# Optimization experiments

Measured on AMD Instinct MI355X. Metric: run time of the kernel, lower is better.

Reference implementation:

```python
import jax, jax.numpy as jnp
import numpy as np
import math

B, T, D = 4, 2048, 1024
N, D_OUT = 1024, 1024
EPS_A = 1e-4
PROJ_BOUND = 1.0


def setup_inputs() -> dict:
    key = jax.random.key(0)
    ks = jax.random.split(key, 4)
    # reset_parameters: rho=0.99, delta0=1.0
    rho, delta0 = 0.99, 1.0
    alpha0 = -math.log(rho) / delta0
    alpha_log_val = math.log(math.expm1(alpha0))
    delta_bias_val = math.log(math.expm1(delta0))
    return {
        "u": jax.random.normal(ks[0], (B, T, D), dtype=jnp.float32),
        "z0": jnp.zeros((B, N), dtype=jnp.float32),
        "W_in_raw": 0.02 * jax.random.normal(ks[1], (N, D), dtype=jnp.float32),
        "W_out_raw": 0.02 * jax.random.normal(ks[2], (D_OUT, N), dtype=jnp.float32),
        "pn_w": 0.02 * jax.random.normal(ks[3], (3 * N, D), dtype=jnp.float32),
        "pn_b": jnp.zeros((3 * N,), dtype=jnp.float32),
        "alpha_log": jnp.full((N,), alpha_log_val, dtype=jnp.float32),
        "delta_bias": jnp.full((N,), delta_bias_val, dtype=jnp.float32),
        "log_gamma": jnp.float32(0.0),
    }


def _bounded_linear(x, W, bound):
    # y = x @ (W/scale)^T with ||W/scale||_2 <= bound (exact spectral norm)
    sigma = jnp.maximum(jnp.linalg.norm(W, ord=2), 1e-5)
    scale = jnp.maximum(sigma / bound, 1.0)
    return x @ (W / scale).T


def reference(u, z0, W_in_raw, W_out_raw, pn_w, pn_b, alpha_log, delta_bias, log_gamma):
    g = jnp.exp(log_gamma)
    u_scaled = g * _bounded_linear(u, W_in_raw, PROJ_BOUND)        # (B,T,N)
    raw = u @ pn_w.T + pn_b                                        # (B,T,3N)
    delta_raw, b_raw, c_raw = jnp.split(raw, 3, axis=-1)
    delta = jax.nn.softplus(delta_raw + delta_bias)
    alpha = jax.nn.softplus(alpha_log)                             # (N,)
    a = jnp.minimum(jnp.exp(-delta * alpha), 1.0 - EPS_A)          # (B,T,N)
    b = jnp.tanh(b_raw)
    c = jnp.tanh(c_raw)
    # exact spectral norm of [[a,b],[c,0]] per coordinate
    p = a * a + c * c
    r = b * b
    q = a * b
    disc = (p - r) * (p - r) + 4.0 * q * q
    lam_max = 0.5 * (p + r + jnp.sqrt(disc + 1e-12))
    sigma = jnp.sqrt(lam_max + 1e-12)
    scale = jnp.maximum(sigma, 1.0)
    a, b, c = a / scale, b / scale, c / scale
    # diagonal recurrence z_{t+1} = a_t * z_t + b_t * u_scaled_t via associative scan
    bu = b * u_scaled
    bu = bu.at[:, 0].add(a[:, 0] * z0)
    def combine(x, y):
        a1, b1 = x
        a2, b2 = y
        return (a2 * a1, a2 * b1 + b2)
    _, z_next = jax.lax.associative_scan(combine, (a, bu), axis=1)  # z_1..z_T (B,T,N)
    # y_t = W_out (c_t * z_t) with z_t = state BEFORE update (one-step delay)
    states = jnp.concatenate([z0[:, None, :], z_next[:, :-1, :]], axis=1)  # z_0..z_{T-1}
    y_hat = c * states
    y = _bounded_linear(y_hat, W_out_raw, PROJ_BOUND)              # (B,T,D_out)
    return y
```

## Files before the change

### kernel.cpp

```cpp
#include <hip/hip_runtime.h>
#include <stdint.h>

#define B_ 4
#define T_ 2048
#define D_ 1024
#define N_ 1024
#define TC 32
#define NCH (T_/TC)
#define SQN 8

typedef __attribute__((ext_vector_type(4))) float f32x4;
typedef __attribute__((ext_vector_type(8))) short bf16x8;
typedef __attribute__((ext_vector_type(4))) unsigned short us4;

__device__ __forceinline__ unsigned short f2bf(float f){
  unsigned int u = __float_as_uint(f);
  return (unsigned short)((u + 0x7fffu + ((u >> 16) & 1u)) >> 16);
}
__device__ __forceinline__ float bf2f(unsigned short h){
  return __uint_as_float(((unsigned int)h) << 16);
}

#define U4    2097152
#define WIN4   262144
#define PNW4   786432
#define WOUT4  262144
#define CONV_BLOCKS ((U4 + WIN4 + PNW4 + WOUT4 + 255)/256)

__global__ void k_convert_all(const float* __restrict__ u, const float* __restrict__ Win,
                              const float* __restrict__ pnw, const float* __restrict__ Wout,
                              unsigned short* __restrict__ u16, unsigned short* __restrict__ Wcat16,
                              unsigned short* __restrict__ Wout16, float* __restrict__ sc){
  if (blockIdx.x == 0 && threadIdx.x < 64) sc[threadIdx.x] = 0.f;
  long i = (long)blockIdx.x * 256 + threadIdx.x;
  const float* src; unsigned short* dst; long o;
  if (i < U4)                      { src = u;    dst = u16;               o = i; }
  else if (i < U4+WIN4)            { src = Win;  dst = Wcat16;            o = i - U4; }
  else if (i < U4+WIN4+PNW4)       { src = pnw;  dst = Wcat16 + 1048576;  o = i - (U4+WIN4); }
  else if (i < U4+WIN4+PNW4+WOUT4) { src = Wout; dst = Wout16;            o = i - (U4+WIN4+PNW4); }
  else return;
  float4 v = ((const float4*)src)[o];
  us4 w;
  w.x = f2bf(v.x); w.y = f2bf(v.y); w.z = f2bf(v.z); w.w = f2bf(v.w);
  ((us4*)dst)[o] = w;
}

__device__ __forceinline__ void load_lds16(const unsigned short* g, unsigned short* l){
  __builtin_amdgcn_global_load_lds((const __attribute__((address_space(1))) void*)g,
                                   (__attribute__((address_space(3))) void*)l, 16, 0, 0);
}

template<int OUTBF16>
__global__ __launch_bounds__(256) void k_gemm(
    const unsigned short* __restrict__ A,
    const unsigned short* __restrict__ Bmat,
    void* __restrict__ C0,
    int M, int N, int K,
    const float* __restrict__ sc, int step)
{
  __shared__ alignas(16) unsigned short As[128*64];
  __shared__ alignas(16) unsigned short Bs[128*64];
  const int tid = threadIdx.x;
  const int wid = tid >> 6;
  const int lane = tid & 63;
  const int bn = blockIdx.x, bm = blockIdx.y;

  char* C = (char*)C0;
  float outscale = (step >= 0) ? sc[step] : 1.f;

  const int wr = wid >> 1, wc = wid & 1;
  const int rg = lane >> 3;
  const int cby = (lane & 7) << 4;
  const int srow0 = wid * 32;
  const int frow = lane & 15;
  const int kgrp = lane >> 4;

  const size_t Abase = (size_t)bm * 128 * K;
  const size_t Bbase = (size_t)bn * 128 * K;

  f32x4 acc[4][4] = {};

  for (int kt = 0; kt < K; kt += 64){
    #pragma unroll
    for (int i = 0; i < 4; i++){
      int r = srow0 + i*8 + rg;
      int cb = cby ^ ((r & 7) << 4);
      load_lds16(A    + Abase + (size_t)r*K + kt + (cb >> 1), As + (srow0 + i*8)*64);
      load_lds16(Bmat + Bbase + (size_t)r*K + kt + (cb >> 1), Bs + (srow0 + i*8)*64);
    }
    __syncthreads();
    #pragma unroll
    for (int kk = 0; kk < 2; kk++){
      const int kbyte = kk*64 + kgrp*16;
      bf16x8 af[4], bfv[4];
      #pragma unroll
      for (int m = 0; m < 4; m++){
        int r = wr*64 + m*16 + frow;
        af[m] = *(const bf16x8*)((const char*)As + r*128 + (kbyte ^ ((r & 7) << 4)));
      }
      #pragma unroll
      for (int n2 = 0; n2 < 4; n2++){
        int r = wc*64 + n2*16 + frow;
        bfv[n2] = *(const bf16x8*)((const char*)Bs + r*128 + (kbyte ^ ((r & 7) << 4)));
      }
      #pragma unroll
      for (int m = 0; m < 4; m++)
        #pragma unroll
        for (int n2 = 0; n2 < 4; n2++)
          acc[m][n2] = __builtin_amdgcn_mfma_f32_16x16x32_bf16(af[m], bfv[n2], acc[m][n2], 0, 0, 0);
    }
    __syncthreads();
  }

  const int row0 = bm*128 + wr*64;
  const int col0 = bn*128 + wc*64 + frow;
  #pragma unroll
  for (int m = 0; m < 4; m++){
    #pragma unroll
    for (int n2 = 0; n2 < 4; n2++){
      const int col = col0 + n2*16;
      const int rb = row0 + m*16 + kgrp*4;
      #pragma unroll
      for (int j = 0; j < 4; j++){
        float v = acc[m][n2][j] * outscale;
        if (OUTBF16) ((unsigned short*)C)[(size_t)(rb + j)*N + col] = f2bf(v);
        else         ((float*)C)[(size_t)(rb + j)*N + col] = v;
      }
    }
  }
}

__global__ __launch_bounds__(256) void k_sq(
    const unsigned short* __restrict__ A0, unsigned short* __restrict__ C0,
    const unsigned short* __restrict__ A1, unsigned short* __restrict__ C1,
    float* __restrict__ sc, int step)
{
  __shared__ alignas(16) unsigned short As0[64*128], Bs0[64*128];
  __shared__ alignas(16) unsigned short As1[64*128], Bs1[64*128];
  const int tid = threadIdx.x;
  const int wid = tid >> 6;
  const int lane = tid & 63;
  const int bn = blockIdx.x, bm = blockIdx.y, z = blockIdx.z;

  const unsigned short* A = z ? A1 : A0;
  unsigned short* C = z ? C1 : C0;
  float outscale = 1.f;
  if (step > 0){ float t = sc[8 + (step-1)*2 + z]; outscale = 1.f/(t*t); }

  const int wr = wid >> 1, wc = wid & 1;
  const int frow = lane & 15;
  const int kgrp = lane >> 4;

  const int srl = lane >> 4;
  const int sgr = lane & 15;
  const int swzr = wid*4 + srl;
  const int scol_e = ((sgr ^ swzr) << 3);

  const size_t Arow = (size_t)bm * 64;
  const size_t Brow = (size_t)bn * 64;

  f32x4 acc[2][2] = {};

  auto stage = [&](unsigned short* as, unsigned short* bs, int t){
    const int kt = t * 128;
    #pragma unroll
    for (int i = 0; i < 4; i++){
      int r = i*16 + wid*4 + srl;
      load_lds16(A + (Arow + r)*1024 + kt + scol_e, as + (i*16 + wid*4)*128);
      load_lds16(A + (Brow + r)*1024 + kt + scol_e, bs + (i*16 + wid*4)*128);
    }
  };

  auto compute = [&](const unsigned short* as, const unsigned short* bs){
    #pragma unroll
    for (int ks = 0; ks < 4; ks++){
      const int kb = ks*64 + kgrp*16;
      bf16x8 af[2], bfv[2];
      #pragma unroll
      for (int m = 0; m < 2; m++){
        int r = wr*32 + m*16 + frow;
        af[m] = *(const bf16x8*)((const char*)as + r*256 + (kb ^ (frow << 4)));
      }
      #pragma unroll
      for (int n2 = 0; n2 < 2; n2++){
        int r = wc*32 + n2*16 + frow;
        bfv[n2] = *(const bf16x8*)((const char*)bs + r*256 + (kb ^ (frow << 4)));
      }
      #pragma unroll
      for (int m = 0; m < 2; m++)
        #pragma unroll
        for (int n2 = 0; n2 < 2; n2++)
          acc[m][n2] = __builtin_amdgcn_mfma_f32_16x16x32_bf16(af[m], bfv[n2], acc[m][n2], 0, 0, 0);
    }
  };

  stage(As0, Bs0, 0);
  __syncthreads();
  for (int t2 = 0; t2 < 8; t2 += 2){
    if (t2 + 1 < 8) stage(As1, Bs1, t2 + 1);
    compute(As0, Bs0);
    __syncthreads();
    if (t2 + 2 < 8) stage(As0, Bs0, t2 + 2);
    compute(As1, Bs1);
    __syncthreads();
  }

  const int row0 = bm*64 + wr*32;
  const int col0 = bn*64 + wc*32 + frow;
  float fr = 0.f;
  #pragma unroll
  for (int m = 0; m < 2; m++){
    #pragma unroll
    for (int n2 = 0; n2 < 2; n2++){
      const int col = col0 + n2*16;
      const int rb = row0 + m*16 + kgrp*4;
      #pragma unroll
      for (int j = 0; j < 4; j++){
        float v = acc[m][n2][j] * outscale;
        C[(size_t)(rb + j)*1024 + col] = f2bf(v);
        fr += v*v;
      }
    }
  }
  if (bm == bn && wr == wc){
    int j = frow - kgrp*4;
    if (j >= 0 && j < 4){
      float d = (acc[0][0][j] + acc[1][1][j]) * outscale;
      atomicAdd(&sc[8 + step*2 + z], d);
    }
  }
  if (step == SQN){
    #pragma unroll
    for (int off = 32; off; off >>= 1) fr += __shfl_down(fr, off, 64);
    if (lane == 0) atomicAdd(&sc[8 + 2*(SQN+1) + z], fr);
  }
}

__global__ void k_final(float* sc){
  int z = threadIdx.x;
  if (z < 2){
    float ll = 0.f, w = 1.f, t = 1.f;
    for (int i = 0; i <= SQN; i++){
      t = sc[8 + 2*i + z];
      ll += w * __logf(t);
      w *= 0.5f;
    }
    float tlast = sc[8 + 2*(SQN+1) + z] / (t*t);
    ll += w * __logf(tlast);
    float sig = __expf(0.5f * ll);
    sig = fmaxf(sig, 1e-5f);
    sc[z] = 1.f / fmaxf(sig, 1.f);
  }
}

__device__ __forceinline__ float softplusf(float x){
  return (x > 0.f) ? (x + __logf(1.f + __expf(-x))) : __logf(1.f + __expf(x));
}
__device__ __forceinline__ float tanhfastf(float x){
  float e = __expf(2.f * x);
  return 1.f - 2.f/(e + 1.f);
}
__device__ __forceinline__ void abc_from(float pin, float draw, float braw, float craw,
    float alpha, float ginv, float& a_o, float& bu_o, float& c_o){
  float sp = softplusf(draw);
  float av = __expf(-sp * alpha);
  av = fminf(av, 1.f - 1e-4f);
  float bv = tanhfastf(braw);
  float cv = tanhfastf(craw);
  float p = av*av + cv*cv;
  float r = bv*bv;
  float q = av*bv;
  float pr = p - r;
  float disc = pr*pr + 4.f*q*q;
  float lam = 0.5f*(p + r + sqrtf(disc + 1e-12f));
  float sig = sqrtf(lam + 1e-12f);
  float inv = 1.f / fmaxf(sig, 1.f);
  a_o = av * inv;
  c_o = cv * inv;
  bu_o = (bv * inv) * (pin * ginv);
}

__global__ __launch_bounds__(256) void k_pass1(
    const unsigned short* __restrict__ P,
    const float* __restrict__ alog, const float* __restrict__ dbias,
    const float* __restrict__ pnb, const float* __restrict__ lgam,
    const float* __restrict__ sc,
    float* __restrict__ Asum, float* __restrict__ Ssum)
{
  const int tid = threadIdx.x;
  const int n0 = blockIdx.y*512 + tid*2;
  const int ch = blockIdx.x, b = blockIdx.z;
  const float ginv = __expf(lgam[0]) * sc[0];
  float alpha[2], bd[2], bb[2], bc[2], A[2], S[2];
  #pragma unroll
  for (int j = 0; j < 2; j++){
    alpha[j] = softplusf(alog[n0+j]);
    bd[j] = dbias[n0+j] + pnb[n0+j];
    bb[j] = pnb[N_ + n0+j];
    bc[j] = pnb[2*N_ + n0+j];
    A[j] = 1.f; S[j] = 0.f;
  }
  const unsigned short* Pr = P + (size_t)(b*T_ + ch*TC) * (4*N_);
  #pragma unroll 4
  for (int i = 0; i < TC; i++){
    unsigned int vp = *(const unsigned int*)(Pr + n0);
    unsigned int vd = *(const unsigned int*)(Pr + N_ + n0);
    unsigned int vb = *(const unsigned int*)(Pr + 2*N_ + n0);
    unsigned int vc = *(const unsigned int*)(Pr + 3*N_ + n0);
    #pragma unroll
    for (int j = 0; j < 2; j++){
      float pin  = bf2f((unsigned short)(j ? (vp>>16) : (vp & 0xffffu)));
      float draw = bf2f((unsigned short)(j ? (vd>>16) : (vd & 0xffffu))) + bd[j];
      float braw = bf2f((unsigned short)(j ? (vb>>16) : (vb & 0xffffu))) + bb[j];
      float craw = bf2f((unsigned short)(j ? (vc>>16) : (vc & 0xffffu))) + bc[j];
      float a, bu, c;
      abc_from(pin, draw, braw, craw, alpha[j], ginv, a, bu, c);
      S[j] = fmaf(a, S[j], bu);
      A[j] *= a;
    }
    Pr += 4*N_;
  }
  const size_t idx = (size_t)(b*NCH + ch)*N_ + n0;
  Asum[idx] = A[0]; Asum[idx+1] = A[1];
  Ssum[idx] = S[0]; Ssum[idx+1] = S[1];
}

__global__ void k_pass2(const float* __restrict__ Asum, const float* __restrict__ Ssum,
                        const float* __restrict__ z0, float* __restrict__ Zent)
{
  const int n = blockIdx.x*256 + threadIdx.x;
  const int b = blockIdx.y;
  float z = z0[b*N_ + n];
  for (int ch = 0; ch < NCH; ch++){
    const size_t idx = (size_t)(b*NCH + ch)*N_ + n;
    Zent[idx] = z;
    z = fmaf(Asum[idx], z, Ssum[idx]);
  }
}

__global__ __launch_bounds__(256) void k_pass3(
    const unsigned short* __restrict__ P,
    const float* __restrict__ alog, const float* __restrict__ dbias,
    const float* __restrict__ pnb, const float* __restrict__ lgam,
    const float* __restrict__ sc, const float* __restrict__ Zent,
    unsigned short* __restrict__ yh)
{
  const int tid = threadIdx.x;
  const int n0 = blockIdx.y*512 + tid*2;
  const int ch = blockIdx.x, b = blockIdx.z;
  const float ginv = __expf(lgam[0]) * sc[0];
  float alpha[2], bd[2], bb[2], bc[2], z[2];
  #pragma unroll
  for (int j = 0; j < 2; j++){
    alpha[j] = softplusf(alog[n0+j]);
    bd[j] = dbias[n0+j] + pnb[n0+j];
    bb[j] = pnb[N_ + n0+j];
    bc[j] = pnb[2*N_ + n0+j];
  }
  const size_t zidx = (size_t)(b*NCH + ch)*N_ + n0;
  z[0] = Zent[zidx]; z[1] = Zent[zidx+1];
  const unsigned short* Pr = P + (size_t)(b*T_ + ch*TC) * (4*N_);
  unsigned short* Y = yh + (size_t)(b*T_ + ch*TC)*N_ + n0;
  #pragma unroll 4
  for (int i = 0; i < TC; i++){
    unsigned int vp = *(const unsigned int*)(Pr + n0);
    unsigned int vd = *(const unsigned int*)(Pr + N_ + n0);
    unsigned int vb = *(const unsigned int*)(Pr + 2*N_ + n0);
    unsigned int vc = *(const unsigned int*)(Pr + 3*N_ + n0);
    unsigned int ow = 0;
    #pragma unroll
    for (int j = 0; j < 2; j++){
      float pin  = bf2f((unsigned short)(j ? (vp>>16) : (vp & 0xffffu)));
      float draw = bf2f((unsigned short)(j ? (vd>>16) : (vd & 0xffffu))) + bd[j];
      float braw = bf2f((unsigned short)(j ? (vb>>16) : (vb & 0xffffu))) + bb[j];
      float craw = bf2f((unsigned short)(j ? (vc>>16) : (vc & 0xffffu))) + bc[j];
      float a, bu, c;
      abc_from(pin, draw, braw, craw, alpha[j], ginv, a, bu, c);
      float yv = c * z[j];
      z[j] = fmaf(a, z[j], bu);
      ow |= ((unsigned int)f2bf(yv)) << (16*j);
    }
    *(unsigned int*)Y = ow;
    Y += N_;
    Pr += 4*N_;
  }
}

extern "C" void kernel_launch(void* const* d_in, const int* in_sizes, int n_in,
                              void* d_out, int out_size, void* d_ws, size_t ws_size,
                              hipStream_t stream)
{
  const float* u    = (const float*)d_in[0];
  const float* z0   = (const float*)d_in[1];
  const float* Win  = (const float*)d_in[2];
  const float* Wout = (const float*)d_in[3];
  const float* pnw  = (const float*)d_in[4];
  const float* pnb  = (const float*)d_in[5];
  const float* alog = (const float*)d_in[6];
  const float* dbias= (const float*)d_in[7];
  const float* lgam = (const float*)d_in[8];

  char* ws = (char*)d_ws;
  size_t off = 0;
  auto alloc = [&](size_t bytes) -> void* {
    void* p = ws + off;
    off += (bytes + 255) & ~(size_t)255;
    return p;
  };
  float*          sc     = (float*)         alloc(1024);
  unsigned short* u16    = (unsigned short*)alloc((size_t)8192*1024*2);
  unsigned short* Wcat16 = (unsigned short*)alloc((size_t)4096*1024*2);
  unsigned short* Wout16 = (unsigned short*)alloc((size_t)1024*1024*2);
  unsigned short* P16    = (unsigned short*)alloc((size_t)8192*4096*2);
  unsigned short* yh16   = (unsigned short*)alloc((size_t)8192*1024*2);
  unsigned short* Hping  = (unsigned short*)alloc((size_t)2*1024*1024*2);
  unsigned short* Hpong  = (unsigned short*)alloc((size_t)2*1024*1024*2);
  float*          Asum   = (float*)alloc((size_t)B_*NCH*N_*4);
  float*          Ssum   = (float*)alloc((size_t)B_*NCH*N_*4);
  float*          Zent   = (float*)alloc((size_t)B_*NCH*N_*4);

  k_convert_all<<<CONV_BLOCKS, 256, 0, stream>>>(u, Win, pnw, Wout, u16, Wcat16, Wout16, sc);

  dim3 gsq(16, 16, 2);
  k_sq<<<gsq, 256, 0, stream>>>(Wcat16, Hping, Wout16, Hping + (size_t)1024*1024, sc, 0);
  unsigned short* hin = Hping;
  unsigned short* hout = Hpong;
  for (int s = 1; s <= SQN; s++){
    k_sq<<<gsq, 256, 0, stream>>>(hin, hout, hin + (size_t)1024*1024, hout + (size_t)1024*1024, sc, s);
    unsigned short* t = hin; hin = hout; hout = t;
  }
  k_final<<<1, 64, 0, stream>>>(sc);

  dim3 g1(4096/128, 8192/128, 1);
  k_gemm<1><<<g1, 256, 0, stream>>>(u16, Wcat16, P16, 8192, 4096, 1024, sc, -1);

  dim3 gp1(NCH, N_/512, B_);
  k_pass1<<<gp1, 256, 0, stream>>>(P16, alog, dbias, pnb, lgam, sc, Asum, Ssum);
  dim3 gp2(N_/256, B_);
  k_pass2<<<gp2, 256, 0, stream>>>(Asum, Ssum, z0, Zent);
  k_pass3<<<gp1, 256, 0, stream>>>(P16, alog, dbias, pnb, lgam, sc, Zent, yh16);

  dim3 g2(1024/128, 8192/128, 1);
  k_gemm<0><<<g2, 256, 0, stream>>>(yh16, Wout16, d_out, 8192, 1024, 1024, sc, 1);
}
```

Baseline: 320.9 us.

## Add 256x256-tile pipelined bf16 GEMM for the input projection

Replaces the generic 128x128 GEMM for the large u @ [W_in; pn_w]^T projection with a dedicated kernel using 256x256 tiles, 512 threads, and a 4-stage LDS ring fed by direct global-to-LDS loads with XOR swizzling. Loads for future k-tiles are interleaved between split MFMA phases, with priority raised around MFMA bursts. The aim is more data reuse per tile and better overlap of memory with compute. It hardcodes K=1024 and an output stride of 4096, no longer applies the scale argument (the old call passed step -1), and uses heavy register and LDS budgets.

After: 332.5 us. 3.6% more time.

```diff
diff --git a/kernel.cpp b/kernel.cpp
--- a/kernel.cpp
+++ b/kernel.cpp
@@ -48,6 +48,132 @@
 __device__ __forceinline__ void load_lds16(const unsigned short* g, unsigned short* l){
   __builtin_amdgcn_global_load_lds((const __attribute__((address_space(1))) void*)g,
                                    (__attribute__((address_space(3))) void*)l, 16, 0, 0);
+}
+
+__global__ __launch_bounds__(512, 2) void k_pgemm(
+    const unsigned short* __restrict__ A,
+    const unsigned short* __restrict__ Bmat,
+    unsigned short* __restrict__ C)
+{
+  __shared__ alignas(16) unsigned short As[4][256*32];
+  __shared__ alignas(16) unsigned short Bs[4][256*32];
+  const int tid = threadIdx.x;
+  const int wid = tid >> 6;
+  const int lane = tid & 63;
+  const int bn = blockIdx.x, bm = blockIdx.y;
+
+  const int wr = wid >> 2;
+  const int wc = wid & 3;
+  const int frow = lane & 15;
+  const int kgrp = lane >> 4;
+
+  const int srow = lane >> 2;
+  const int sgr  = lane & 3;
+
+  f32x4 acc[8][4] = {};
+
+  const unsigned short* Ab = A + (size_t)bm * 256 * 1024;
+  const unsigned short* Bb = Bmat + (size_t)bn * 256 * 1024;
+
+  auto stageA = [&](int t){
+    const int p = t & 3;
+    #pragma unroll
+    for (int l = 0; l < 2; l++){
+      int r = (wid*2 + l)*16 + srow;
+      int g = sgr ^ ((r >> 1) & 3);
+      load_lds16(Ab + (size_t)r*1024 + t*32 + g*8, &As[p][(wid*2 + l)*512]);
+    }
+  };
+  auto stageB = [&](int t){
+    const int p = t & 3;
+    #pragma unroll
+    for (int l = 0; l < 2; l++){
+      int r = (wid*2 + l)*16 + srow;
+      int g = sgr ^ ((r >> 1) & 3);
+      load_lds16(Bb + (size_t)r*1024 + t*32 + g*8, &Bs[p][(wid*2 + l)*512]);
+    }
+  };
+
+  stageA(0); stageB(0);
+  stageA(1); stageB(1);
+  stageA(2); stageB(2);
+  asm volatile("s_waitcnt vmcnt(8)" ::: "memory");
+  __builtin_amdgcn_s_barrier();
+
+  bf16x8 bfv[4];
+
+  auto tile_body = [&](int t, bool doStage){
+    const int p = t & 3;
+    bf16x8 afv[4];
+    #pragma unroll
+    for (int m = 0; m < 4; m++){
+      int r = wr*128 + m*16 + frow;
+      int g = kgrp ^ ((r >> 1) & 3);
+      afv[m] = *(const bf16x8*)&As[p][r*32 + g*8];
+    }
+    #pragma unroll
+    for (int n = 0; n < 4; n++){
+      int r = wc*64 + n*16 + frow;
+      int g = kgrp ^ ((r >> 1) & 3);
+      bfv[n] = *(const bf16x8*)&Bs[p][r*32 + g*8];
+    }
+    if (doStage) stageA(t + 3);
+    __builtin_amdgcn_s_barrier();
+    asm volatile("s_waitcnt lgkmcnt(0)" ::: "memory");
+    __builtin_amdgcn_sched_barrier(0);
+    __builtin_amdgcn_s_setprio(1);
+    #pragma unroll
+    for (int m = 0; m < 4; m++)
+      #pragma unroll
+      for (int n = 0; n < 4; n++)
+        acc[m][n] = __builtin_amdgcn_mfma_f32_16x16x32_bf16(afv[m], bfv[n], acc[m][n], 0, 0, 0);
+    __builtin_amdgcn_s_setprio(0);
+    __builtin_amdgcn_s_barrier();
+    #pragma unroll
+    for (int m = 0; m < 4; m++){
+      int r = wr*128 + (m+4)*16 + frow;
+      int g = kgrp ^ ((r >> 1) & 3);
+      afv[m] = *(const bf16x8*)&As[p][r*32 + g*8];
+    }
+    if (doStage) stageB(t + 3);
+    __builtin_amdgcn_s_barrier();
+    asm volatile("s_waitcnt lgkmcnt(0)" ::: "memory");
+    __builtin_amdgcn_sched_barrier(0);
+    __builtin_amdgcn_s_setprio(1);
+    #pragma unroll
+    for (int m = 0; m < 4; m++)
+      #pragma unroll
+      for (int n = 0; n < 4; n++)
+        acc[m+4][n] = __builtin_amdgcn_mfma_f32_16x16x32_bf16(afv[m], bfv[n], acc[m+4][n], 0, 0, 0);
+    __builtin_amdgcn_s_setprio(0);
+  };
+
+  for (int t = 0; t < 29; t++){
+    tile_body(t, true);
+    asm volatile("s_waitcnt vmcnt(8)" ::: "memory");
+    __builtin_amdgcn_s_barrier();
+  }
+  tile_body(29, false);
+  asm volatile("s_waitcnt vmcnt(4)" ::: "memory");
+  __builtin_amdgcn_s_barrier();
+  tile_body(30, false);
+  asm volatile("s_waitcnt vmcnt(0)" ::: "memory");
+  __builtin_amdgcn_s_barrier();
+  tile_body(31, false);
+
+  const int row0 = bm*256 + wr*128;
+  const int col0 = bn*256 + wc*64 + frow;
+  #pragma unroll
+  for (int m = 0; m < 8; m++){
+    #pragma unroll
+    for (int n = 0; n < 4; n++){
+      const int col = col0 + n*16;
+      const int rb = row0 + m*16 + kgrp*4;
+      #pragma unroll
+      for (int j = 0; j < 4; j++)
+        C[(size_t)(rb + j)*4096 + col] = f2bf(acc[m][n][j]);
+    }
+  }
 }
 
 template<int OUTBF16>
@@ -431,8 +557,8 @@
   }
   k_final<<<1, 64, 0, stream>>>(sc);
 
-  dim3 g1(4096/128, 8192/128, 1);
-  k_gemm<1><<<g1, 256, 0, stream>>>(u16, Wcat16, P16, 8192, 4096, 1024, sc, -1);
+  dim3 gP(4096/256, 8192/256);
+  k_pgemm<<<gP, 512, 0, stream>>>(u16, Wcat16, P16);
 
   dim3 gp1(NCH, N_/512, B_);
   k_pass1<<<gp1, 256, 0, stream>>>(P16, alog, dbias, pnb, lgam, sc, Asum, Ssum);
@@ -440,6 +566,6 @@
   k_pass2<<<gp2, 256, 0, stream>>>(Asum, Ssum, z0, Zent);
   k_pass3<<<gp1, 256, 0, stream>>>(P16, alog, dbias, pnb, lgam, sc, Zent, yh16);
 
-  dim3 g2(1024/128, 8192/128, 1);
+  dim3 g2(1024/128, 8192/128);
   k_gemm<0><<<g2, 256, 0, stream>>>(yh16, Wout16, d_out, 8192, 1024, 1024, sc, 1);
 }
```

## Fuse squaring chain and scan tail into persistent kernels with grid barriers

Applied to the files above, without the earlier changes.

Replaces the nine per-step squaring launches and the k_final launch with one persistent 512-block kernel. The steps inside it are separated by a software grid barrier built on an atomic counter. The three scan passes and the output GEMM are likewise merged into one 512-block kernel with grid barriers between phases. The goal is to remove kernel launch gaps and tail effects. In exchange it relies on all 512 blocks being co-resident, spin-waits on atomics, and runs the output GEMM inside the tail kernel rather than as a separate tuned launch.

Result: slower. 1.216 ms (+278.8%).

```diff
diff --git a/kernel.cpp b/kernel.cpp
--- a/kernel.cpp
+++ b/kernel.cpp
@@ -21,6 +21,18 @@
   return __uint_as_float(((unsigned int)h) << 16);
 }
 
+__device__ __forceinline__ void gsync(unsigned* bar, unsigned target){
+  __syncthreads();
+  if (threadIdx.x == 0){
+    __threadfence();
+    atomicAdd(bar, 1u);
+    while (__hip_atomic_load(bar, __ATOMIC_ACQUIRE, __HIP_MEMORY_SCOPE_AGENT) < target)
+      __builtin_amdgcn_s_sleep(2);
+    __threadfence();
+  }
+  __syncthreads();
+}
+
 #define U4    2097152
 #define WIN4   262144
 #define PNW4   786432
@@ -31,7 +43,7 @@
                               const float* __restrict__ pnw, const float* __restrict__ Wout,
                               unsigned short* __restrict__ u16, unsigned short* __restrict__ Wcat16,
                               unsigned short* __restrict__ Wout16, float* __restrict__ sc){
-  if (blockIdx.x == 0 && threadIdx.x < 64) sc[threadIdx.x] = 0.f;
+  if (blockIdx.x == 0 && threadIdx.x < 128) sc[threadIdx.x] = 0.f;
   long i = (long)blockIdx.x * 256 + threadIdx.x;
   const float* src; unsigned short* dst; long o;
   if (i < U4)                      { src = u;    dst = u16;               o = i; }
@@ -130,126 +142,133 @@
   }
 }
 
-__global__ __launch_bounds__(256) void k_sq(
-    const unsigned short* __restrict__ A0, unsigned short* __restrict__ C0,
-    const unsigned short* __restrict__ A1, unsigned short* __restrict__ C1,
-    float* __restrict__ sc, int step)
+__global__ __launch_bounds__(256) void k_chain(
+    const unsigned short* __restrict__ W0,
+    const unsigned short* __restrict__ W1,
+    unsigned short* __restrict__ Hp,
+    unsigned short* __restrict__ Hq,
+    float* sc, unsigned* bar)
 {
   __shared__ alignas(16) unsigned short As0[64*128], Bs0[64*128];
   __shared__ alignas(16) unsigned short As1[64*128], Bs1[64*128];
   const int tid = threadIdx.x;
   const int wid = tid >> 6;
   const int lane = tid & 63;
-  const int bn = blockIdx.x, bm = blockIdx.y, z = blockIdx.z;
-
-  const unsigned short* A = z ? A1 : A0;
-  unsigned short* C = z ? C1 : C0;
-  float outscale = 1.f;
-  if (step > 0){ float t = sc[8 + (step-1)*2 + z]; outscale = 1.f/(t*t); }
+  const int bid = blockIdx.x;
+  const int z  = bid >> 8;
+  const int bm = (bid >> 4) & 15, bn = bid & 15;
+  const size_t M2 = (size_t)1024*1024;
 
   const int wr = wid >> 1, wc = wid & 1;
   const int frow = lane & 15;
   const int kgrp = lane >> 4;
-
   const int srl = lane >> 4;
   const int sgr = lane & 15;
   const int swzr = wid*4 + srl;
   const int scol_e = ((sgr ^ swzr) << 3);
-
   const size_t Arow = (size_t)bm * 64;
   const size_t Brow = (size_t)bn * 64;
 
-  f32x4 acc[2][2] = {};
-
-  auto stage = [&](unsigned short* as, unsigned short* bs, int t){
-    const int kt = t * 128;
+  for (int step = 0; step <= SQN; step++){
+    const unsigned short* A = (step == 0) ? (z ? W1 : W0)
+                             : (((step & 1) ? Hp : Hq) + (z ? M2 : 0));
+    unsigned short* C = ((step & 1) ? Hq : Hp) + (z ? M2 : 0);
+    float outscale = 1.f;
+    if (step > 0){
+      float t = __hip_atomic_load(&sc[8 + (step-1)*2 + z], __ATOMIC_ACQUIRE, __HIP_MEMORY_SCOPE_AGENT);
+      outscale = 1.f / (t*t);
+    }
+
+    f32x4 acc[2][2] = {};
+
+    auto stage = [&](unsigned short* as, unsigned short* bs, int t2){
+      const int kt = t2 * 128;
+      #pragma unroll
+      for (int i = 0; i < 4; i++){
+        int r = i*16 + wid*4 + srl;
+        load_lds16(A + (Arow + r)*1024 + kt + scol_e, as + (i*16 + wid*4)*128);
+        load_lds16(A + (Brow + r)*1024 + kt + scol_e, bs + (i*16 + wid*4)*128);
+      }
+    };
+    auto compute = [&](const unsigned short* as, const unsigned short* bs){
+      #pragma unroll
+      for (int ks = 0; ks < 4; ks++){
+        const int kb = ks*64 + kgrp*16;
+        bf16x8 af[2], bfv[2];
+        #pragma unroll
+        for (int m = 0; m < 2; m++){
+          int r = wr*32 + m*16 + frow;
+          af[m] = *(const bf16x8*)((const char*)as + r*256 + (kb ^ (frow << 4)));
+        }
+        #pragma unroll
+        for (int n2 = 0; n2 < 2; n2++){
+          int r = wc*32 + n2*16 + frow;
+          bfv[n2] = *(const bf16x8*)((const char*)bs + r*256 + (kb ^ (frow << 4)));
+        }
+        #pragma unroll
+        for (int m = 0; m < 2; m++)
+          #pragma unroll
+          for (int n2 = 0; n2 < 2; n2++)
+            acc[m][n2] = __builtin_amdgcn_mfma_f32_16x16x32_bf16(af[m], bfv[n2], acc[m][n2], 0, 0, 0);
+      }
+    };
+
+    stage(As0, Bs0, 0);
+    __syncthreads();
+    for (int t2 = 0; t2 < 8; t2 += 2){
+      if (t2 + 1 < 8) stage(As1, Bs1, t2 + 1);
+      compute(As0, Bs0);
+      __syncthreads();
+      if (t2 + 2 < 8) stage(As0, Bs0, t2 + 2);
+      compute(As1, Bs1);
+      __syncthreads();
+    }
+
+    const int row0 = bm*64 + wr*32;
+    const int col0 = bn*64 + wc*32 + frow;
+    float fr = 0.f;
     #pragma unroll
-    for (int i = 0; i < 4; i++){
-      int r = i*16 + wid*4 + srl;
-      load_lds16(A + (Arow + r)*1024 + kt + scol_e, as + (i*16 + wid*4)*128);
-      load_lds16(A + (Brow + r)*1024 + kt + scol_e, bs + (i*16 + wid*4)*128);
-    }
-  };
-
-  auto compute = [&](const unsigned short* as, const unsigned short* bs){
-    #pragma unroll
-    for (int ks = 0; ks < 4; ks++){
-      const int kb = ks*64 + kgrp*16;
-      bf16x8 af[2], bfv[2];
-      #pragma unroll
-      for (int m = 0; m < 2; m++){
-        int r = wr*32 + m*16 + frow;
-        af[m] = *(const bf16x8*)((const char*)as + r*256 + (kb ^ (frow << 4)));
-      }
+    for (int m = 0; m < 2; m++){
       #pragma unroll
       for (int n2 = 0; n2 < 2; n2++){
-        int r = wc*32 + n2*16 + frow;
-        bfv[n2] = *(const bf16x8*)((const char*)bs + r*256 + (kb ^ (frow << 4)));
-      }
-      #pragma unroll
-      for (int m = 0; m < 2; m++)
-        #pragma unroll
-        for (int n2 = 0; n2 < 2; n2++)
-          acc[m][n2] = __builtin_amdgcn_mfma_f32_16x16x32_bf16(af[m], bfv[n2], acc[m][n2], 0, 0, 0);
-    }
-  };
-
-  stage(As0, Bs0, 0);
-  __syncthreads();
-  for (int t2 = 0; t2 < 8; t2 += 2){
-    if (t2 + 1 < 8) stage(As1, Bs1, t2 + 1);
-    compute(As0, Bs0);
-    __syncthreads();
-    if (t2 + 2 < 8) stage(As0, Bs0, t2 + 2);
-    compute(As1, Bs1);
-    __syncthreads();
-  }
-
-  const int row0 = bm*64 + wr*32;
-  const int col0 = bn*64 + wc*32 + frow;
-  float fr = 0.f;
-  #pragma unroll
-  for (int m = 0; m < 2; m++){
-    #pragma unroll
-    for (int n2 = 0; n2 < 2; n2++){
-      const int col = col0 + n2*16;
-      const int rb = row0 + m*16 + kgrp*4;
-      #pragma unroll
-      for (int j = 0; j < 4; j++){
-        float v = acc[m][n2][j] * outscale;
-        C[(size_t)(rb + j)*1024 + col] = f2bf(v);
-        fr += v*v;
-      }
-    }
-  }
-  if (bm == bn && wr == wc){
-    int j = frow - kgrp*4;
-    if (j >= 0 && j < 4){
-      float d = (acc[0][0][j] + acc[1][1][j]) * outscale;
-      atomicAdd(&sc[8 + step*2 + z], d);
-    }
-  }
-  if (step == SQN){
-    #pragma unroll
-    for (int off = 32; off; off >>= 1) fr += __shfl_down(fr, off, 64);
-    if (lane == 0) atomicAdd(&sc[8 + 2*(SQN+1) + z], fr);
-  }
-}
-
-__global__ void k_final(float* sc){
-  int z = threadIdx.x;
-  if (z < 2){
+        const int col = col0 + n2*16;
+        const int rb = row0 + m*16 + kgrp*4;
+        #pragma unroll
+        for (int j = 0; j < 4; j++){
+          float v = acc[m][n2][j] * outscale;
+          C[(size_t)(rb + j)*1024 + col] = f2bf(v);
+          fr += v*v;
+        }
+      }
+    }
+    if (bm == bn && wr == wc){
+      int j = frow - kgrp*4;
+      if (j >= 0 && j < 4){
+        float d = (acc[0][0][j] + acc[1][1][j]) * outscale;
+        atomicAdd(&sc[8 + step*2 + z], d);
+      }
+    }
+    if (step == SQN){
+      #pragma unroll
+      for (int off = 32; off; off >>= 1) fr += __shfl_down(fr, off, 64);
+      if (lane == 0) atomicAdd(&sc[8 + 2*(SQN+1) + z], fr);
+    }
+    gsync(bar, (unsigned)((step + 1) * 512));
+  }
+
+  if (bid == 0 && tid < 2){
+    const int zz = tid;
     float ll = 0.f, w = 1.f, t = 1.f;
     for (int i = 0; i <= SQN; i++){
-      t = sc[8 + 2*i + z];
+      t = __hip_atomic_load(&sc[8 + 2*i + zz], __ATOMIC_RELAXED, __HIP_MEMORY_SCOPE_AGENT);
       ll += w * __logf(t);
       w *= 0.5f;
     }
-    float tlast = sc[8 + 2*(SQN+1) + z] / (t*t);
-    ll += w * __logf(tlast);
+    float F = __hip_atomic_load(&sc[8 + 2*(SQN+1) + zz], __ATOMIC_RELAXED, __HIP_MEMORY_SCOPE_AGENT);
+    ll += w * __logf(F / (t*t));
     float sig = __expf(0.5f * ll);
     sig = fmaxf(sig, 1e-5f);
-    sc[z] = 1.f / fmaxf(sig, 1.f);
+    sc[zz] = 1.f / fmaxf(sig, 1.f);
   }
 }
 
@@ -280,109 +299,166 @@
   bu_o = (bv * inv) * (pin * ginv);
 }
 
-__global__ __launch_bounds__(256) void k_pass1(
+__global__ __launch_bounds__(256) void k_tail(
     const unsigned short* __restrict__ P,
     const float* __restrict__ alog, const float* __restrict__ dbias,
     const float* __restrict__ pnb, const float* __restrict__ lgam,
-    const float* __restrict__ sc,
-    float* __restrict__ Asum, float* __restrict__ Ssum)
+    const float* __restrict__ sc, const float* __restrict__ z0,
+    float* __restrict__ Asum, float* __restrict__ Ssum, float* __restrict__ Zent,
+    unsigned short* __restrict__ yh,
+    const unsigned short* __restrict__ Wout16, float* __restrict__ dout,
+    unsigned* bar)
 {
+  __shared__ alignas(16) unsigned short As[128*64];
+  __shared__ alignas(16) unsigned short Bs[128*64];
   const int tid = threadIdx.x;
-  const int n0 = blockIdx.y*512 + tid*2;
-  const int ch = blockIdx.x, b = blockIdx.z;
+  const int bid = blockIdx.x;
+
+  const int ch = bid & 63, ny = (bid >> 6) & 1, pb = bid >> 7;
+  const int n0 = ny*512 + tid*2;
   const float ginv = __expf(lgam[0]) * sc[0];
-  float alpha[2], bd[2], bb[2], bc[2], A[2], S[2];
+  float alpha[2], bd[2], bb[2], bc[2];
   #pragma unroll
   for (int j = 0; j < 2; j++){
     alpha[j] = softplusf(alog[n0+j]);
     bd[j] = dbias[n0+j] + pnb[n0+j];
     bb[j] = pnb[N_ + n0+j];
     bc[j] = pnb[2*N_ + n0+j];
-    A[j] = 1.f; S[j] = 0.f;
-  }
-  const unsigned short* Pr = P + (size_t)(b*T_ + ch*TC) * (4*N_);
-  #pragma unroll 4
-  for (int i = 0; i < TC; i++){
-    unsigned int vp = *(const unsigned int*)(Pr + n0);
-    unsigned int vd = *(const unsigned int*)(Pr + N_ + n0);
-    unsigned int vb = *(const unsigned int*)(Pr + 2*N_ + n0);
-    unsigned int vc = *(const unsigned int*)(Pr + 3*N_ + n0);
+  }
+
+  {
+    float A[2] = {1.f, 1.f}, S[2] = {0.f, 0.f};
+    const unsigned short* Pr = P + (size_t)(pb*T_ + ch*TC) * (4*N_);
+    #pragma unroll 4
+    for (int i = 0; i < TC; i++){
+      unsigned int vp = *(const unsigned int*)(Pr + n0);
+      unsigned int vd = *(const unsigned int*)(Pr + N_ + n0);
+      unsigned int vb = *(const unsigned int*)(Pr + 2*N_ + n0);
+      unsigned int vc = *(const unsigned int*)(Pr + 3*N_ + n0);
+      #pragma unroll
+      for (int j = 0; j < 2; j++){
+        float pin  = bf2f((unsigned short)(j ? (vp>>16) : (vp & 0xffffu)));
+        float draw = bf2f((unsigned short)(j ? (vd>>16) : (vd & 0xffffu))) + bd[j];
+        float braw = bf2f((unsigned short)(j ? (vb>>16) : (vb & 0xffffu))) + bb[j];
+        float craw = bf2f((unsigned short)(j ? (vc>>16) : (vc & 0xffffu))) + bc[j];
+        float a, bu, c;
+        abc_from(pin, draw, braw, craw, alpha[j], ginv, a, bu, c);
+        S[j] = fmaf(a, S[j], bu);
+        A[j] *= a;
+      }
+      Pr += 4*N_;
+    }
+    const size_t idx = (size_t)(pb*NCH + ch)*N_ + n0;
+    Asum[idx] = A[0]; Asum[idx+1] = A[1];
+    Ssum[idx] = S[0]; Ssum[idx+1] = S[1];
+  }
+  gsync(bar, 512u);
+
+  if (bid < 16){
+    const int n = (bid & 3)*256 + tid;
+    const int b2 = bid >> 2;
+    float zv = z0[b2*N_ + n];
+    for (int c2 = 0; c2 < NCH; c2++){
+      const size_t idx = (size_t)(b2*NCH + c2)*N_ + n;
+      Zent[idx] = zv;
+      zv = fmaf(Asum[idx], zv, Ssum[idx]);
+    }
+  }
+  gsync(bar, 1024u);
+
+  {
+    float zr[2];
+    const size_t zidx = (size_t)(pb*NCH + ch)*N_ + n0;
+    zr[0] = Zent[zidx]; zr[1] = Zent[zidx+1];
+    const unsigned short* Pr = P + (size_t)(pb*T_ + ch*TC) * (4*N_);
+    unsigned short* Y = yh + (size_t)(pb*T_ + ch*TC)*N_ + n0;
+    #pragma unroll 4
+    for (int i = 0; i < TC; i++){
+      unsigned int vp = *(const unsigned int*)(Pr + n0);
+      unsigned int vd = *(const unsigned int*)(Pr + N_ + n0);
+      unsigned int vb = *(const unsigned int*)(Pr + 2*N_ + n0);
+      unsigned int vc = *(const unsigned int*)(Pr + 3*N_ + n0);
+      unsigned int ow = 0;
+      #pragma unroll
+      for (int j = 0; j < 2; j++){
+        float pin  = bf2f((unsigned short)(j ? (vp>>16) : (vp & 0xffffu)));
+        float draw = bf2f((unsigned short)(j ? (vd>>16) : (vd & 0xffffu))) + bd[j];
+        float braw = bf2f((unsigned short)(j ? (vb>>16) : (vb & 0xffffu))) + bb[j];
+        float craw = bf2f((unsigned short)(j ? (vc>>16) : (vc & 0xffffu))) + bc[j];
+        float a, bu, c;
+        abc_from(pin, draw, braw, craw, alpha[j], ginv, a, bu, c);
+        float yv = c * zr[j];
+        zr[j] = fmaf(a, zr[j], bu);
+        ow |= ((unsigned int)f2bf(yv)) << (16*j);
+      }
+      *(unsigned int*)Y = ow;
+      Y += N_;
+      Pr += 4*N_;
+    }
+  }
+  gsync(bar, 1536u);
+
+  {
+    const int bn = bid & 7, bm = bid >> 3;
+    const int wid = tid >> 6;
+    const int lane = tid & 63;
+    const float outscale = sc[1];
+    const int wr = wid >> 1, wc = wid & 1;
+    const int rg = lane >> 3;
+    const int cby = (lane & 7) << 4;
+    const int srow0 = wid * 32;
+    const int frow = lane & 15;
+    const int kgrp = lane >> 4;
+    const size_t Abase = (size_t)bm * 128 * 1024;
+    const size_t Bbase = (size_t)bn * 128 * 1024;
+
+    f32x4 acc[4][4] = {};
+
+    for (int kt = 0; kt < 1024; kt += 64){
+      #pragma unroll
+      for (int i = 0; i < 4; i++){
+        int r = srow0 + i*8 + rg;
+        int cb = cby ^ ((r & 7) << 4);
+        load_lds16(yh     + Abase + (size_t)r*1024 + kt + (cb >> 1), As + (srow0 + i*8)*64);
+        load_lds16(Wout16 + Bbase + (size_t)r*1024 + kt + (cb >> 1), Bs + (srow0 + i*8)*64);
+      }
+      __syncthreads();
+      #pragma unroll
+      for (int kk = 0; kk < 2; kk++){
+        const int kbyte = kk*64 + kgrp*16;
+        bf16x8 af[4], bfv[4];
+        #pragma unroll
+        for (int m = 0; m < 4; m++){
+          int r = wr*64 + m*16 + frow;
+          af[m] = *(const bf16x8*)((const char*)As + r*128 + (kbyte ^ ((r & 7) << 4)));
+        }
+        #pragma unroll
+        for (int n2 = 0; n2 < 4; n2++){
+          int r = wc*64 + n2*16 + frow;
+          bfv[n2] = *(const bf16x8*)((const char*)Bs + r*128 + (kbyte ^ ((r & 7) << 4)));
+        }
+        #pragma unroll
+        for (int m = 0; m < 4; m++)
+          #pragma unroll
+          for (int n2 = 0; n2 < 4; n2++)
+            acc[m][n2] = __builtin_amdgcn_mfma_f32_16x16x32_bf16(af[m], bfv[n2], acc[m][n2], 0, 0, 0);
+      }
+      __syncthreads();
+    }
+
+    const int row0 = bm*128 + wr*64;
+    const int col0 = bn*128 + wc*64 + frow;
     #pragma unroll
-    for (int j = 0; j < 2; j++){
-      float pin  = bf2f((unsigned short)(j ? (vp>>16) : (vp & 0xffffu)));
-      float draw = bf2f((unsigned short)(j ? (vd>>16) : (vd & 0xffffu))) + bd[j];
-      float braw = bf2f((unsigned short)(j ? (vb>>16) : (vb & 0xffffu))) + bb[j];
-      float craw = bf2f((unsigned short)(j ? (vc>>16) : (vc & 0xffffu))) + bc[j];
-      float a, bu, c;
-      abc_from(pin, draw, braw, craw, alpha[j], ginv, a, bu, c);
-      S[j] = fmaf(a, S[j], bu);
-      A[j] *= a;
-    }
-    Pr += 4*N_;
-  }
-  const size_t idx = (size_t)(b*NCH + ch)*N_ + n0;
-  Asum[idx] = A[0]; Asum[idx+1] = A[1];
-  Ssum[idx] = S[0]; Ssum[idx+1] = S[1];
-}
-
-__global__ void k_pass2(const float* __restrict__ Asum, const float* __restrict__ Ssum,
-                        const float* __restrict__ z0, float* __restrict__ Zent)
-{
-  const int n = blockIdx.x*256 + threadIdx.x;
-  const int b = blockIdx.y;
-  float z = z0[b*N_ + n];
-  for (int ch = 0; ch < NCH; ch++){
-    const size_t idx = (size_t)(b*NCH + ch)*N_ + n;
-    Zent[idx] = z;
-    z = fmaf(Asum[idx], z, Ssum[idx]);
-  }
-}
-
-__global__ __launch_bounds__(256) void k_pass3(
-    const unsigned short* __restrict__ P,
-    const float* __restrict__ alog, const float* __restrict__ dbias,
-    const float* __restrict__ pnb, const float* __restrict__ lgam,
-    const float* __restrict__ sc, const float* __restrict__ Zent,
-    unsigned short* __restrict__ yh)
-{
-  const int tid = threadIdx.x;
-  const int n0 = blockIdx.y*512 + tid*2;
-  const int ch = blockIdx.x, b = blockIdx.z;
-  const float ginv = __expf(lgam[0]) * sc[0];
-  float alpha[2], bd[2], bb[2], bc[2], z[2];
-  #pragma unroll
-  for (int j = 0; j < 2; j++){
-    alpha[j] = softplusf(alog[n0+j]);
-    bd[j] = dbias[n0+j] + pnb[n0+j];
-    bb[j] = pnb[N_ + n0+j];
-    bc[j] = pnb[2*N_ + n0+j];
-  }
-  const size_t zidx = (size_t)(b*NCH + ch)*N_ + n0;
-  z[0] = Zent[zidx]; z[1] = Zent[zidx+1];
-  const unsigned short* Pr = P + (size_t)(b*T_ + ch*TC) * (4*N_);
-  unsigned short* Y = yh + (size_t)(b*T_ + ch*TC)*N_ + n0;
-  #pragma unroll 4
-  for (int i = 0; i < TC; i++){
-    unsigned int vp = *(const unsigned int*)(Pr + n0);
-    unsigned int vd = *(const unsigned int*)(Pr + N_ + n0);
-    unsigned int vb = *(const unsigned int*)(Pr + 2*N_ + n0);
-    unsigned int vc = *(const unsigned int*)(Pr + 3*N_ + n0);
-    unsigned int ow = 0;
-    #pragma unroll
-    for (int j = 0; j < 2; j++){
-      float pin  = bf2f((unsigned short)(j ? (vp>>16) : (vp & 0xffffu)));
-      float draw = bf2f((unsigned short)(j ? (vd>>16) : (vd & 0xffffu))) + bd[j];
-      float braw = bf2f((unsigned short)(j ? (vb>>16) : (vb & 0xffffu))) + bb[j];
-      float craw = bf2f((unsigned short)(j ? (vc>>16) : (vc & 0xffffu))) + bc[j];
-      float a, bu, c;
-      abc_from(pin, draw, braw, craw, alpha[j], ginv, a, bu, c);
-      float yv = c * z[j];
-      z[j] = fmaf(a, z[j], bu);
-      ow |= ((unsigned int)f2bf(yv)) << (16*j);
-    }
-    *(unsigned int*)Y = ow;
-    Y += N_;
-    Pr += 4*N_;
+    for (int m = 0; m < 4; m++){
+      #pragma unroll
+      for (int n2 = 0; n2 < 4; n2++){
+        const int col = col0 + n2*16;
+        const int rb = row0 + m*16 + kgrp*4;
+        #pragma unroll
+        for (int j = 0; j < 4; j++)
+          dout[(size_t)(rb + j)*1024 + col] = acc[m][n2][j] * outscale;
+      }
+    }
   }
 }
 
@@ -419,27 +495,16 @@
   float*          Ssum   = (float*)alloc((size_t)B_*NCH*N_*4);
   float*          Zent   = (float*)alloc((size_t)B_*NCH*N_*4);
 
+  unsigned* barc = (unsigned*)(sc + 64);
+  unsigned* bart = (unsigned*)(sc + 80);
+
   k_convert_all<<<CONV_BLOCKS, 256, 0, stream>>>(u, Win, pnw, Wout, u16, Wcat16, Wout16, sc);
 
-  dim3 gsq(16, 16, 2);
-  k_sq<<<gsq, 256, 0, stream>>>(Wcat16, Hping, Wout16, Hping + (size_t)1024*1024, sc, 0);
-  unsigned short* hin = Hping;
-  unsigned short* hout = Hpong;
-  for (int s = 1; s <= SQN; s++){
-    k_sq<<<gsq, 256, 0, stream>>>(hin, hout, hin + (size_t)1024*1024, hout + (size_t)1024*1024, sc, s);
-    unsigned short* t = hin; hin = hout; hout = t;
-  }
-  k_final<<<1, 64, 0, stream>>>(sc);
-
-  dim3 g1(4096/128, 8192/128, 1);
+  k_chain<<<512, 256, 0, stream>>>(Wcat16, Wout16, Hping, Hpong, sc, barc);
+
+  dim3 g1(4096/128, 8192/128);
   k_gemm<1><<<g1, 256, 0, stream>>>(u16, Wcat16, P16, 8192, 4096, 1024, sc, -1);
 
-  dim3 gp1(NCH, N_/512, B_);
-  k_pass1<<<gp1, 256, 0, stream>>>(P16, alog, dbias, pnb, lgam, sc, Asum, Ssum);
-  dim3 gp2(N_/256, B_);
-  k_pass2<<<gp2, 256, 0, stream>>>(Asum, Ssum, z0, Zent);
-  k_pass3<<<gp1, 256, 0, stream>>>(P16, alog, dbias, pnb, lgam, sc, Zent, yh16);
-
-  dim3 g2(1024/128, 8192/128, 1);
-  k_gemm<0><<<g2, 256, 0, stream>>>(yh16, Wout16, d_out, 8192, 1024, 1024, sc, 1);
-}
+  k_tail<<<512, 256, 0, stream>>>(P16, alog, dbias, pnb, lgam, sc, z0,
+                                  Asum, Ssum, Zent, yh16, Wout16, (float*)d_out, bart);
+}
```

## Inline spectral scale, widen scan threads to four columns, shorten chunks and squarings

Applied to the files above, without the earlier changes.

Drops the separate k_final launch: each consumer now recomputes the spectral-norm inverse scale from the accumulated statistics through an inlined helper. The scan passes handle four columns per thread with 8-byte vector loads and stores instead of two, and the chunk length is halved so the grid keeps enough blocks. The number of repeated-squaring steps drops from 8 to 7, which saves one squaring GEMM launch but makes the spectral-norm estimate less accurate. Shorter chunks also make pass2's sequential loop twice as long and add more Asum/Ssum/Zent traffic.

Result: faster. 314.3 us (-2.1%).

```diff
diff --git a/kernel.cpp b/kernel.cpp
--- a/kernel.cpp
+++ b/kernel.cpp
@@ -5,9 +5,9 @@
 #define T_ 2048
 #define D_ 1024
 #define N_ 1024
-#define TC 32
+#define TC 16
 #define NCH (T_/TC)
-#define SQN 8
+#define SQN 7
 
 typedef __attribute__((ext_vector_type(4))) float f32x4;
 typedef __attribute__((ext_vector_type(8))) short bf16x8;
@@ -19,6 +19,20 @@
 }
 __device__ __forceinline__ float bf2f(unsigned short h){
   return __uint_as_float(((unsigned int)h) << 16);
+}
+
+__device__ __forceinline__ float inv_scale(const float* __restrict__ sc, int z){
+  float ll = 0.f, w = 1.f, t = 1.f;
+  #pragma unroll
+  for (int i = 0; i <= SQN; i++){
+    t = sc[8 + 2*i + z];
+    ll += w * __logf(t);
+    w *= 0.5f;
+  }
+  float F = sc[8 + 2*(SQN+1) + z];
+  ll += w * __logf(F / (t*t));
+  float sig = fmaxf(__expf(0.5f * ll), 1e-5f);
+  return 1.f / fmaxf(sig, 1.f);
 }
 
 #define U4    2097152
@@ -66,7 +80,7 @@
   const int bn = blockIdx.x, bm = blockIdx.y;
 
   char* C = (char*)C0;
-  float outscale = (step >= 0) ? sc[step] : 1.f;
+  float outscale = (step >= 0) ? inv_scale(sc, step) : 1.f;
 
   const int wr = wid >> 1, wc = wid & 1;
   const int rg = lane >> 3;
@@ -233,23 +247,6 @@
     #pragma unroll
     for (int off = 32; off; off >>= 1) fr += __shfl_down(fr, off, 64);
     if (lane == 0) atomicAdd(&sc[8 + 2*(SQN+1) + z], fr);
-  }
-}
-
-__global__ void k_final(float* sc){
-  int z = threadIdx.x;
-  if (z < 2){
-    float ll = 0.f, w = 1.f, t = 1.f;
-    for (int i = 0; i <= SQN; i++){
-      t = sc[8 + 2*i + z];
-      ll += w * __logf(t);
-      w *= 0.5f;
-    }
-    float tlast = sc[8 + 2*(SQN+1) + z] / (t*t);
-    ll += w * __logf(tlast);
-    float sig = __expf(0.5f * ll);
-    sig = fmaxf(sig, 1e-5f);
-    sc[z] = 1.f / fmaxf(sig, 1.f);
   }
 }
 
@@ -288,12 +285,12 @@
     float* __restrict__ Asum, float* __restrict__ Ssum)
 {
   const int tid = threadIdx.x;
-  const int n0 = blockIdx.y*512 + tid*2;
-  const int ch = blockIdx.x, b = blockIdx.z;
-  const float ginv = __expf(lgam[0]) * sc[0];
-  float alpha[2], bd[2], bb[2], bc[2], A[2], S[2];
-  #pragma unroll
-  for (int j = 0; j < 2; j++){
+  const int n0 = tid*4;
+  const int ch = blockIdx.x, b = blockIdx.y;
+  const float ginv = __expf(lgam[0]) * inv_scale(sc, 0);
+  float alpha[4], bd[4], bb[4], bc[4], A[4], S[4];
+  #pragma unroll
+  for (int j = 0; j < 4; j++){
     alpha[j] = softplusf(alog[n0+j]);
     bd[j] = dbias[n0+j] + pnb[n0+j];
     bb[j] = pnb[N_ + n0+j];
@@ -301,28 +298,25 @@
     A[j] = 1.f; S[j] = 0.f;
   }
   const unsigned short* Pr = P + (size_t)(b*T_ + ch*TC) * (4*N_);
-  #pragma unroll 4
+  #pragma unroll 2
   for (int i = 0; i < TC; i++){
-    unsigned int vp = *(const unsigned int*)(Pr + n0);
-    unsigned int vd = *(const unsigned int*)(Pr + N_ + n0);
-    unsigned int vb = *(const unsigned int*)(Pr + 2*N_ + n0);
-    unsigned int vc = *(const unsigned int*)(Pr + 3*N_ + n0);
-    #pragma unroll
-    for (int j = 0; j < 2; j++){
-      float pin  = bf2f((unsigned short)(j ? (vp>>16) : (vp & 0xffffu)));
-      float draw = bf2f((unsigned short)(j ? (vd>>16) : (vd & 0xffffu))) + bd[j];
-      float braw = bf2f((unsigned short)(j ? (vb>>16) : (vb & 0xffffu))) + bb[j];
-      float craw = bf2f((unsigned short)(j ? (vc>>16) : (vc & 0xffffu))) + bc[j];
+    us4 vp = *(const us4*)(Pr + n0);
+    us4 vd = *(const us4*)(Pr + N_ + n0);
+    us4 vb = *(const us4*)(Pr + 2*N_ + n0);
+    us4 vc = *(const us4*)(Pr + 3*N_ + n0);
+    #pragma unroll
+    for (int j = 0; j < 4; j++){
       float a, bu, c;
-      abc_from(pin, draw, braw, craw, alpha[j], ginv, a, bu, c);
+      abc_from(bf2f(vp[j]), bf2f(vd[j]) + bd[j], bf2f(vb[j]) + bb[j], bf2f(vc[j]) + bc[j],
+               alpha[j], ginv, a, bu, c);
       S[j] = fmaf(a, S[j], bu);
       A[j] *= a;
     }
     Pr += 4*N_;
   }
   const size_t idx = (size_t)(b*NCH + ch)*N_ + n0;
-  Asum[idx] = A[0]; Asum[idx+1] = A[1];
-  Ssum[idx] = S[0]; Ssum[idx+1] = S[1];
+  #pragma unroll
+  for (int j = 0; j < 4; j++){ Asum[idx+j] = A[j]; Ssum[idx+j] = S[j]; }
 }
 
 __global__ void k_pass2(const float* __restrict__ Asum, const float* __restrict__ Ssum,
@@ -346,41 +340,39 @@
     unsigned short* __restrict__ yh)
 {
   const int tid = threadIdx.x;
-  const int n0 = blockIdx.y*512 + tid*2;
-  const int ch = blockIdx.x, b = blockIdx.z;
-  const float ginv = __expf(lgam[0]) * sc[0];
-  float alpha[2], bd[2], bb[2], bc[2], z[2];
-  #pragma unroll
-  for (int j = 0; j < 2; j++){
+  const int n0 = tid*4;
+  const int ch = blockIdx.x, b = blockIdx.y;
+  const float ginv = __expf(lgam[0]) * inv_scale(sc, 0);
+  float alpha[4], bd[4], bb[4], bc[4], z[4];
+  #pragma unroll
+  for (int j = 0; j < 4; j++){
     alpha[j] = softplusf(alog[n0+j]);
     bd[j] = dbias[n0+j] + pnb[n0+j];
     bb[j] = pnb[N_ + n0+j];
     bc[j] = pnb[2*N_ + n0+j];
   }
   const size_t zidx = (size_t)(b*NCH + ch)*N_ + n0;
-  z[0] = Zent[zidx]; z[1] = Zent[zidx+1];
+  #pragma unroll
+  for (int j = 0; j < 4; j++) z[j] = Zent[zidx+j];
   const unsigned short* Pr = P + (size_t)(b*T_ + ch*TC) * (4*N_);
   unsigned short* Y = yh + (size_t)(b*T_ + ch*TC)*N_ + n0;
-  #pragma unroll 4
+  #pragma unroll 2
   for (int i = 0; i < TC; i++){
-    unsigned int vp = *(const unsigned int*)(Pr + n0);
-    unsigned int vd = *(const unsigned int*)(Pr + N_ + n0);
-    unsigned int vb = *(const unsigned int*)(Pr + 2*N_ + n0);
-    unsigned int vc = *(const unsigned int*)(Pr + 3*N_ + n0);
-    unsigned int ow = 0;
-    #pragma unroll
-    for (int j = 0; j < 2; j++){
-      float pin  = bf2f((unsigned short)(j ? (vp>>16) : (vp & 0xffffu)));
-      float draw = bf2f((unsigned short)(j ? (vd>>16) : (vd & 0xffffu))) + bd[j];
-      float braw = bf2f((unsigned short)(j ? (vb>>16) : (vb & 0xffffu))) + bb[j];
-      float craw = bf2f((unsigned short)(j ? (vc>>16) : (vc & 0xffffu))) + bc[j];
+    us4 vp = *(const us4*)(Pr + n0);
+    us4 vd = *(const us4*)(Pr + N_ + n0);
+    us4 vb = *(const us4*)(Pr + 2*N_ + n0);
+    us4 vc = *(const us4*)(Pr + 3*N_ + n0);
+    us4 ow;
+    #pragma unroll
+    for (int j = 0; j < 4; j++){
       float a, bu, c;
-      abc_from(pin, draw, braw, craw, alpha[j], ginv, a, bu, c);
+      abc_from(bf2f(vp[j]), bf2f(vd[j]) + bd[j], bf2f(vb[j]) + bb[j], bf2f(vc[j]) + bc[j],
+               alpha[j], ginv, a, bu, c);
       float yv = c * z[j];
       z[j] = fmaf(a, z[j], bu);
-      ow |= ((unsigned int)f2bf(yv)) << (16*j);
-    }
-    *(unsigned int*)Y = ow;
+      ow[j] = f2bf(yv);
+    }
+    *(us4*)Y = ow;
     Y += N_;
     Pr += 4*N_;
   }
@@ -429,17 +421,16 @@
     k_sq<<<gsq, 256, 0, stream>>>(hin, hout, hin + (size_t)1024*1024, hout + (size_t)1024*1024, sc, s);
     unsigned short* t = hin; hin = hout; hout = t;
   }
-  k_final<<<1, 64, 0, stream>>>(sc);
-
-  dim3 g1(4096/128, 8192/128, 1);
+
+  dim3 g1(4096/128, 8192/128);
   k_gemm<1><<<g1, 256, 0, stream>>>(u16, Wcat16, P16, 8192, 4096, 1024, sc, -1);
 
-  dim3 gp1(NCH, N_/512, B_);
+  dim3 gp1(NCH, B_);
   k_pass1<<<gp1, 256, 0, stream>>>(P16, alog, dbias, pnb, lgam, sc, Asum, Ssum);
   dim3 gp2(N_/256, B_);
   k_pass2<<<gp2, 256, 0, stream>>>(Asum, Ssum, z0, Zent);
   k_pass3<<<gp1, 256, 0, stream>>>(P16, alog, dbias, pnb, lgam, sc, Zent, yh16);
 
-  dim3 g2(1024/128, 8192/128, 1);
+  dim3 g2(1024/128, 8192/128);
   k_gemm<0><<<g2, 256, 0, stream>>>(yh16, Wout16, d_out, 8192, 1024, 1024, sc, 1);
 }
```
